# Kernel optimization log

Hardware: AMD Instinct MI355X
Metric: run time of the kernel (lower is better)

The kernel has to match this reference:

```python
import jax, jax.numpy as jnp
import numpy as np

THRESHOLD = 0.2
NEG_POS_RATIO = 3
ALPHA = 1.0
B, M, P, C = 64, 50, 24564, 2


def cxcy_to_xy(c):
    return jnp.concatenate([c[..., :2] - c[..., 2:] / 2, c[..., :2] + c[..., 2:] / 2], axis=-1)


def xy_to_cxcy(x):
    return jnp.concatenate([(x[..., :2] + x[..., 2:]) / 2, x[..., 2:] - x[..., :2]], axis=-1)


def cxcy_to_gcxgcy(c, p):
    # SSD encoding: offsets scaled by 10, sizes (log) scaled by 5
    return jnp.concatenate([(c[..., :2] - p[..., :2]) / (p[..., 2:] / 10.0),
                            jnp.log(c[..., 2:] / p[..., 2:]) * 5.0], axis=-1)


def jaccard(a, b):
    # a: (M,4) xy boxes, b: (P,4) xy boxes -> (M,P) IoU
    lt = jnp.maximum(a[:, None, :2], b[None, :, :2])
    rb = jnp.minimum(a[:, None, 2:], b[None, :, 2:])
    inter = jnp.prod(jnp.clip(rb - lt, 0.0), axis=-1)
    area_a = jnp.prod(a[:, 2:] - a[:, :2], axis=-1)
    area_b = jnp.prod(b[:, 2:] - b[:, :2], axis=-1)
    return inter / (area_a[:, None] + area_b[None, :] - inter)


def setup_inputs() -> dict:
    key = jax.random.key(0)
    k1, k2, k3, k4, k5, k6 = jax.random.split(key, 6)
    predicted_locs = jax.random.normal(k1, (B, P, 4), dtype=jnp.float32)
    predicted_scores = jax.random.normal(k2, (B, P, C), dtype=jnp.float32)
    # valid GT corner boxes in [0,1]: x2>x1, y2>y1
    xy1 = jax.random.uniform(k3, (B, M, 2), minval=0.0, maxval=0.75)
    wh = jax.random.uniform(k4, (B, M, 2), minval=0.05, maxval=0.25)
    boxes = jnp.concatenate([xy1, xy1 + wh], axis=-1).astype(jnp.float32)
    # priors in cxcywh with positive sizes
    pc = jax.random.uniform(k5, (P, 2), minval=0.0, maxval=1.0)
    pwh = jax.random.uniform(k6, (P, 2), minval=0.02, maxval=0.3)
    priors_cxcy = jnp.concatenate([pc, pwh], axis=-1).astype(jnp.float32)
    return {"predicted_locs": predicted_locs, "predicted_scores": predicted_scores,
            "boxes": boxes, "priors_cxcy": priors_cxcy}


def reference(predicted_locs, predicted_scores, boxes, priors_cxcy):
    n_priors = priors_cxcy.shape[0]
    priors_xy = cxcy_to_xy(priors_cxcy)

    def assign(boxes_i):  # boxes_i: (M,4) xy
        overlap = jaccard(boxes_i, priors_xy)  # (M,P)
        overlap_for_each_prior = overlap.max(axis=0)        # (P,)
        object_for_each_prior = overlap.argmax(axis=0)      # (P,)
        prior_for_each_object = overlap.argmax(axis=1)      # (M,)
        # force each object's best prior to be assigned to that object
        object_for_each_prior = object_for_each_prior.at[prior_for_each_object].set(jnp.arange(boxes_i.shape[0]))
        overlap_for_each_prior = overlap_for_each_prior.at[prior_for_each_object].set(1.0)
        labels = jnp.where(overlap_for_each_prior < THRESHOLD, 0, 1).astype(jnp.int32)
        true_locs = cxcy_to_gcxgcy(xy_to_cxcy(boxes_i[object_for_each_prior]), priors_cxcy)
        return labels, true_locs

    true_classes, true_locs = jax.vmap(assign)(boxes)  # (B,P), (B,P,4)
    pos = true_classes != 0                            # (B,P)
    n_pos = pos.sum(axis=1)                            # (B,)
    total_pos = n_pos.sum().astype(jnp.float32)

    # L1Loss(mean) over the positive-prior coordinates
    loc_abs = jnp.abs(predicted_locs - true_locs)
    loc_loss = jnp.sum(loc_abs * pos[..., None]) / (total_pos * 4.0)

    # per-prior cross entropy
    logp = jax.nn.log_softmax(predicted_scores, axis=-1)
    conf_all = -jnp.take_along_axis(logp, true_classes[..., None].astype(jnp.int32), axis=-1)[..., 0]  # (B,P)
    conf_pos_sum = jnp.sum(conf_all * pos)

    # hard negative mining: zero positives, sort descending, take top 3*n_pos per image
    conf_neg = jnp.where(pos, 0.0, conf_all)
    conf_neg_sorted = -jnp.sort(-conf_neg, axis=1)
    ranks = jnp.arange(n_priors)[None, :]
    hard = ranks < (NEG_POS_RATIO * n_pos)[:, None]
    conf_hard_sum = jnp.sum(conf_neg_sorted * hard)

    conf_loss = (conf_hard_sum + conf_pos_sum) / total_pos
    return conf_loss + ALPHA * loc_loss
```

## Files before the change

### kernel.cpp

```cpp
#include <hip/hip_runtime.h>
#include <math.h>

#define BB 64
#define MM 50
#define PP 24564
#define CC 2
#define NBLK ((PP + 255) / 256)
#define THRESH 0.2f
#define P4 (PP / 4)
#define MCH 5
#define MGRID (MM / MCH)

__global__ void k_priors(const float4* __restrict__ pr_cxcy,
                         float4* __restrict__ pr_xy,
                         float* __restrict__ parea,
                         int* __restrict__ ghist) {
    int p = blockIdx.x * 256 + threadIdx.x;
    for (int i = p; i < BB * 2048; i += NBLK * 256) ghist[i] = 0;
    if (p >= PP) return;
    float4 c = pr_cxcy[p];
    float4 xy;
    xy.x = c.x - c.z * 0.5f;
    xy.y = c.y - c.w * 0.5f;
    xy.z = c.x + c.z * 0.5f;
    xy.w = c.y + c.w * 0.5f;
    pr_xy[p] = xy;
    parea[p] = (xy.z - xy.x) * (xy.w - xy.y);
}

__global__ void k_best_per_object(const float4* __restrict__ pr_xy,
                                  const float* __restrict__ parea,
                                  const float4* __restrict__ boxes,
                                  int* __restrict__ pfeo) {
    int b = blockIdx.y;
    int m0 = blockIdx.x * MCH;
    int tid = threadIdx.x;
    float4 bx[MCH];
    float ba[MCH];
    #pragma unroll
    for (int j = 0; j < MCH; ++j) {
        bx[j] = boxes[b * MM + m0 + j];
        ba[j] = (bx[j].z - bx[j].x) * (bx[j].w - bx[j].y);
    }
    float bi[MCH], bd[MCH];
    int bp[MCH];
    #pragma unroll
    for (int j = 0; j < MCH; ++j) { bi[j] = 0.0f; bd[j] = 1.0f; bp[j] = 0; }
    for (int p = tid; p < PP; p += 256) {
        float4 pxy = pr_xy[p];
        float pa = parea[p];
        #pragma unroll
        for (int j = 0; j < MCH; ++j) {
            float lx = fmaxf(bx[j].x, pxy.x), ly = fmaxf(bx[j].y, pxy.y);
            float rx = fminf(bx[j].z, pxy.z), ry = fminf(bx[j].w, pxy.w);
            float iw = fmaxf(rx - lx, 0.0f), ih = fmaxf(ry - ly, 0.0f);
            float inter = iw * ih;
            float den = ba[j] + pa - inter;
            float l = inter * bd[j], r = bi[j] * den;
            if (l > r) { bi[j] = inter; bd[j] = den; bp[j] = p; }
        }
    }
    __shared__ float sI[256], sD[256];
    __shared__ int sP[256];
    for (int j = 0; j < MCH; ++j) {
        sI[tid] = bi[j]; sD[tid] = bd[j]; sP[tid] = bp[j];
        __syncthreads();
        for (int s = 128; s > 0; s >>= 1) {
            if (tid < s) {
                float l = sI[tid + s] * sD[tid], r = sI[tid] * sD[tid + s];
                if (l > r || (l == r && sP[tid + s] < sP[tid])) {
                    sI[tid] = sI[tid + s]; sD[tid] = sD[tid + s]; sP[tid] = sP[tid + s];
                }
            }
            __syncthreads();
        }
        if (tid == 0) pfeo[b * MM + m0 + j] = sP[0];
        __syncthreads();
    }
}

__global__ void k_fused(const float4* __restrict__ pr_xy,
                        const float* __restrict__ parea,
                        const float4* __restrict__ boxes,
                        const int* __restrict__ pfeo,
                        const float4* __restrict__ pr_cxcy,
                        const float4* __restrict__ plocs,
                        const float2* __restrict__ scores,
                        float* __restrict__ confneg,
                        int* __restrict__ ghist,
                        int* __restrict__ npos_part,
                        float* __restrict__ cpos_part,
                        float* __restrict__ loc_part) {
    int b = blockIdx.y;
    int p = blockIdx.x * 256 + threadIdx.x;
    int tid = threadIdx.x;
    __shared__ float4 sbox[MM];
    __shared__ float sarea[MM];
    __shared__ int spfeo[MM];
    __shared__ int shist[2048];
    __shared__ int si[256];
    __shared__ float s1[256], s2[256];
    for (int i = tid; i < 2048; i += 256) shist[i] = 0;
    if (tid < MM) {
        float4 bx = boxes[b * MM + tid];
        sbox[tid] = bx;
        sarea[tid] = (bx.z - bx.x) * (bx.w - bx.y);
        spfeo[tid] = pfeo[b * MM + tid];
    }
    __syncthreads();

    int np = 0;
    float cpos = 0.0f, lloc = 0.0f;
    if (p < PP) {
        float4 pxy = pr_xy[p];
        float pa = parea[p];
        float binter = 0.0f, bdenom = 1.0f;
        int bm = 0;
        for (int m = 0; m < MM; ++m) {
            float4 bxm = sbox[m];
            float lx = fmaxf(bxm.x, pxy.x), ly = fmaxf(bxm.y, pxy.y);
            float rx = fminf(bxm.z, pxy.z), ry = fminf(bxm.w, pxy.w);
            float iw = fmaxf(rx - lx, 0.0f), ih = fmaxf(ry - ly, 0.0f);
            float inter = iw * ih;
            float den = sarea[m] + pa - inter;
            float l = inter * bdenom, r = binter * den;
            if (l > r) { binter = inter; bdenom = den; bm = m; }
        }
        float best = binter / bdenom;
        for (int m = 0; m < MM; ++m) {
            if (spfeo[m] == p) { bm = m; best = 1.0f; }
        }
        bool pos = (best >= THRESH);
        size_t idx = (size_t)b * PP + p;
        float2 sc = scores[idx];
        float mx = fmaxf(sc.x, sc.y);
        float lse = mx + logf(expf(sc.x - mx) + expf(sc.y - mx));
        float conf = pos ? (lse - sc.y) : (lse - sc.x);
        float key = pos ? 0.0f : conf;
        confneg[idx] = key;
        atomicAdd(&shist[__float_as_uint(key) >> 20], 1);
        if (pos) {
            np = 1;
            cpos = conf;
            float4 bx = sbox[bm];
            float cx = (bx.x + bx.z) * 0.5f, cy = (bx.y + bx.w) * 0.5f;
            float w = bx.z - bx.x, h = bx.w - bx.y;
            float4 pc = pr_cxcy[p];
            float g0 = (cx - pc.x) / (pc.z * 0.1f);
            float g1 = (cy - pc.y) / (pc.w * 0.1f);
            float g2 = logf(w / pc.z) * 5.0f;
            float g3 = logf(h / pc.w) * 5.0f;
            float4 pl = plocs[idx];
            lloc = fabsf(pl.x - g0) + fabsf(pl.y - g1) +
                   fabsf(pl.z - g2) + fabsf(pl.w - g3);
        }
    }
    si[tid] = np; s1[tid] = cpos; s2[tid] = lloc;
    __syncthreads();
    for (int s = 128; s > 0; s >>= 1) {
        if (tid < s) {
            si[tid] += si[tid + s];
            s1[tid] += s1[tid + s];
            s2[tid] += s2[tid + s];
        }
        __syncthreads();
    }
    if (tid == 0) {
        int o = b * NBLK + blockIdx.x;
        npos_part[o] = si[0];
        cpos_part[o] = s1[0];
        loc_part[o] = s2[0];
    }
    for (int i = tid; i < 2048; i += 256) {
        int c = shist[i];
        if (c) atomicAdd(&ghist[b * 2048 + i], c);
    }
}

__device__ __forceinline__ float block_sum(float v, float* fred, int tid) {
    fred[tid] = v;
    __syncthreads();
    for (int s = 128; s > 0; s >>= 1) {
        if (tid < s) fred[tid] += fred[tid + s];
        __syncthreads();
    }
    float r = fred[0];
    __syncthreads();
    return r;
}

template <int NB>
__device__ __forceinline__ void suffix_find(const int* __restrict__ h, int K, int tid,
                                            int* iscr, int* bcast, int slot) {
    const int c = NB / 256;
    const int base = tid * c;
    int tsum = 0;
    #pragma unroll
    for (int i = 0; i < c; ++i) tsum += h[base + i];
    iscr[tid] = tsum;
    __syncthreads();
    int val = tsum;
    for (int off = 1; off < 256; off <<= 1) {
        int other = (tid + off < 256) ? iscr[tid + off] : 0;
        __syncthreads();
        val += other;
        iscr[tid] = val;
        __syncthreads();
    }
    int acc = val - tsum;
    int best = -1, cg = 0;
    for (int i = base + c - 1; i >= base; --i) {
        int s = acc + h[i];
        if (s >= K) { best = i; cg = acc; break; }
        acc = s;
    }
    iscr[tid] = best;
    __syncthreads();
    for (int s2 = 128; s2 > 0; s2 >>= 1) {
        if (tid < s2) iscr[tid] = max(iscr[tid], iscr[tid + s2]);
        __syncthreads();
    }
    int gbest = iscr[0];
    __syncthreads();
    if (best == gbest && best >= 0) { bcast[slot] = gbest; bcast[slot + 1] = cg; }
    __syncthreads();
}

__global__ void k_select(const float* __restrict__ confneg,
                         const int* __restrict__ ghist,
                         const int* __restrict__ npos_part,
                         float* __restrict__ chard) {
    int b = blockIdx.x, tid = threadIdx.x;
    __shared__ int h[2048];
    __shared__ float store[4096];
    __shared__ float fred[256];
    __shared__ int iscr[256];
    __shared__ int bcast[8];

    iscr[tid] = (tid < NBLK) ? npos_part[b * NBLK + tid] : 0;
    __syncthreads();
    for (int s = 128; s > 0; s >>= 1) {
        if (tid < s) iscr[tid] += iscr[tid + s];
        __syncthreads();
    }
    int npos = iscr[0];
    __syncthreads();
    long long Kl = 3LL * npos;
    int K = (Kl > PP) ? PP : (int)Kl;
    if (K == 0) {
        if (tid == 0) chard[b] = 0.0f;
        return;
    }

    for (int i = tid; i < 2048; i += 256) h[i] = ghist[b * 2048 + i];
    __syncthreads();
    suffix_find<2048>(h, K, tid, iscr, bcast, 0);
    int b1 = bcast[0];
    int K1 = K - bcast[1];
    int h1cnt = h[b1];
    bool docollect = (h1cnt <= 4096);
    __syncthreads();

    for (int i = tid; i < 1024; i += 256) h[i] = 0;
    if (tid == 0) bcast[6] = 0;
    __syncthreads();
    const float4* cn4 = (const float4*)(confneg + (size_t)b * PP);
    float sa = 0.0f;
    for (int i = tid; i < P4; i += 256) {
        float4 q = cn4[i];
        float vv[4] = {q.x, q.y, q.z, q.w};
        #pragma unroll
        for (int j = 0; j < 4; ++j) {
            unsigned k = __float_as_uint(vv[j]);
            int t11 = (int)(k >> 20);
            if (t11 > b1) sa += vv[j];
            else if (t11 == b1) {
                atomicAdd(&h[(k >> 10) & 1023], 1);
                if (docollect) {
                    int ix = atomicAdd(&bcast[6], 1);
                    store[ix] = vv[j];
                }
            }
        }
    }
    float Sa = block_sum(sa, fred, tid);
    suffix_find<1024>(h, K1, tid, iscr, bcast, 2);
    int b2 = bcast[2];
    int K2 = K1 - bcast[3];
    unsigned top21 = ((unsigned)b1 << 10) | (unsigned)b2;
    __syncthreads();

    float Sb, Sc;
    int b3, K3;
    if (docollect) {
        for (int i = tid; i < 1024; i += 256) h[i] = 0;
        __syncthreads();
        float sb = 0.0f;
        for (int i = tid; i < h1cnt; i += 256) {
            unsigned k = __float_as_uint(store[i]);
            int n10 = (int)((k >> 10) & 1023);
            if (n10 > b2) sb += store[i];
            else if (n10 == b2) atomicAdd(&h[k & 1023], 1);
        }
        Sb = block_sum(sb, fred, tid);
        suffix_find<1024>(h, K2, tid, iscr, bcast, 4);
        b3 = bcast[4];
        K3 = K2 - bcast[5];
        float sc = 0.0f;
        for (int i = tid; i < h1cnt; i += 256) {
            unsigned k = __float_as_uint(store[i]);
            if ((k >> 10) == top21 && (k & 1023) > (unsigned)b3) sc += store[i];
        }
        Sc = block_sum(sc, fred, tid);
    } else {
        for (int i = tid; i < 1024; i += 256) h[i] = 0;
        __syncthreads();
        float sb = 0.0f;
        for (int i = tid; i < P4; i += 256) {
            float4 q = cn4[i];
            float vv[4] = {q.x, q.y, q.z, q.w};
            #pragma unroll
            for (int j = 0; j < 4; ++j) {
                unsigned k = __float_as_uint(vv[j]);
                if ((int)(k >> 20) == b1) {
                    int n10 = (int)((k >> 10) & 1023);
                    if (n10 > b2) sb += vv[j];
                    else if (n10 == b2) atomicAdd(&h[k & 1023], 1);
                }
            }
        }
        Sb = block_sum(sb, fred, tid);
        suffix_find<1024>(h, K2, tid, iscr, bcast, 4);
        b3 = bcast[4];
        K3 = K2 - bcast[5];
        float sc = 0.0f;
        for (int i = tid; i < P4; i += 256) {
            float4 q = cn4[i];
            float vv[4] = {q.x, q.y, q.z, q.w};
            #pragma unroll
            for (int j = 0; j < 4; ++j) {
                unsigned k = __float_as_uint(vv[j]);
                if ((k >> 10) == top21 && (k & 1023) > (unsigned)b3) sc += vv[j];
            }
        }
        Sc = block_sum(sc, fred, tid);
    }
    if (tid == 0) {
        unsigned kstar = (top21 << 10) | (unsigned)b3;
        chard[b] = Sa + Sb + Sc + (float)K3 * __uint_as_float(kstar);
    }
}

__global__ void k_final(const int* __restrict__ npos_part,
                        const float* __restrict__ cpos_part,
                        const float* __restrict__ loc_part,
                        const float* __restrict__ chard,
                        float* __restrict__ out) {
    __shared__ int si[256];
    __shared__ float s1[256], s2[256], s3[256];
    int tn = 0; float tc = 0.0f, tl = 0.0f;
    for (int i = threadIdx.x; i < BB * NBLK; i += 256) {
        tn += npos_part[i];
        tc += cpos_part[i];
        tl += loc_part[i];
    }
    float th = (threadIdx.x < BB) ? chard[threadIdx.x] : 0.0f;
    si[threadIdx.x] = tn; s1[threadIdx.x] = tc; s2[threadIdx.x] = tl; s3[threadIdx.x] = th;
    __syncthreads();
    for (int s = 128; s > 0; s >>= 1) {
        if (threadIdx.x < s) {
            si[threadIdx.x] += si[threadIdx.x + s];
            s1[threadIdx.x] += s1[threadIdx.x + s];
            s2[threadIdx.x] += s2[threadIdx.x + s];
            s3[threadIdx.x] += s3[threadIdx.x + s];
        }
        __syncthreads();
    }
    if (threadIdx.x == 0) {
        float tp = (float)si[0];
        out[0] = (s3[0] + s1[0]) / tp + s2[0] / (tp * 4.0f);
    }
}

extern "C" void kernel_launch(void* const* d_in, const int* in_sizes, int n_in,
                              void* d_out, int out_size, void* d_ws, size_t ws_size,
                              hipStream_t stream) {
    const float4* plocs   = (const float4*)d_in[0];
    const float2* scores  = (const float2*)d_in[1];
    const float4* boxes   = (const float4*)d_in[2];
    const float4* priors  = (const float4*)d_in[3];
    float* out = (float*)d_out;

    char* ws = (char*)d_ws;
    size_t off = 0;
    auto alloc = [&](size_t bytes) -> void* {
        void* p = ws + off;
        off += (bytes + 255) & ~(size_t)255;
        return p;
    };
    float4* pr_xy    = (float4*)alloc((size_t)PP * 16);
    float*  parea    = (float*) alloc((size_t)PP * 4);
    int*    pfeo     = (int*)   alloc((size_t)BB * MM * 4);
    float*  confneg  = (float*) alloc((size_t)BB * PP * 4);
    int*    ghist    = (int*)   alloc((size_t)BB * 2048 * 4);
    int*    npos_p   = (int*)   alloc((size_t)BB * NBLK * 4);
    float*  cpos_p   = (float*) alloc((size_t)BB * NBLK * 4);
    float*  loc_p    = (float*) alloc((size_t)BB * NBLK * 4);
    float*  chard    = (float*) alloc((size_t)BB * 4);
    (void)ws_size; (void)in_sizes; (void)n_in; (void)out_size;

    k_priors<<<dim3(NBLK), 256, 0, stream>>>(priors, pr_xy, parea, ghist);
    k_best_per_object<<<dim3(MGRID, BB), 256, 0, stream>>>(pr_xy, parea, boxes, pfeo);
    k_fused<<<dim3(NBLK, BB), 256, 0, stream>>>(pr_xy, parea, boxes, pfeo, priors,
                                                plocs, scores, confneg, ghist,
                                                npos_p, cpos_p, loc_p);
    k_select<<<BB, 256, 0, stream>>>(confneg, ghist, npos_p, chard);
    k_final<<<1, 256, 0, stream>>>(npos_p, cpos_p, loc_p, chard, out);
}
```

Measured before the change: 160.3 us.

## Split best-prior-per-object search across prior chunks with packed 64-bit atomicMax

Splits the argmax over priors for each ground-truth object into 8 prior chunks across a new grid dimension, giving more blocks. Each block reduces within a wavefront using shuffles and merges partial winners with a 64-bit atomicMax on a key of (IoU bits, inverted prior index). The shared-memory tree reduction and its barriers go away, and each block now handles 10 objects instead of 5. The per-wave atomic merge relies on the IoU being computed by division, which can differ slightly from the cross-multiplied comparison and change tie handling. The key buffer is zeroed in the prior kernel.

```diff
diff --git a/kernel.cpp b/kernel.cpp
--- a/kernel.cpp
+++ b/kernel.cpp
@@ -8,15 +8,19 @@
 #define NBLK ((PP + 255) / 256)
 #define THRESH 0.2f
 #define P4 (PP / 4)
-#define MCH 5
+#define MCH 10
 #define MGRID (MM / MCH)
+#define NC 8
+#define PCHUNK ((PP + NC - 1) / NC)
 
 __global__ void k_priors(const float4* __restrict__ pr_cxcy,
                          float4* __restrict__ pr_xy,
                          float* __restrict__ parea,
-                         int* __restrict__ ghist) {
+                         int* __restrict__ ghist,
+                         unsigned long long* __restrict__ pfeo64) {
     int p = blockIdx.x * 256 + threadIdx.x;
     for (int i = p; i < BB * 2048; i += NBLK * 256) ghist[i] = 0;
+    if (p < BB * MM) pfeo64[p] = 0ull;
     if (p >= PP) return;
     float4 c = pr_cxcy[p];
     float4 xy;
@@ -31,10 +35,13 @@
 __global__ void k_best_per_object(const float4* __restrict__ pr_xy,
                                   const float* __restrict__ parea,
                                   const float4* __restrict__ boxes,
-                                  int* __restrict__ pfeo) {
-    int b = blockIdx.y;
+                                  unsigned long long* __restrict__ pfeo64) {
+    int b = blockIdx.z;
     int m0 = blockIdx.x * MCH;
+    int c = blockIdx.y;
     int tid = threadIdx.x;
+    int pstart = c * PCHUNK;
+    int pend = min(pstart + PCHUNK, PP);
     float4 bx[MCH];
     float ba[MCH];
     #pragma unroll
@@ -46,7 +53,7 @@
     int bp[MCH];
     #pragma unroll
     for (int j = 0; j < MCH; ++j) { bi[j] = 0.0f; bd[j] = 1.0f; bp[j] = 0; }
-    for (int p = tid; p < PP; p += 256) {
+    for (int p = pstart + tid; p < pend; p += 256) {
         float4 pxy = pr_xy[p];
         float pa = parea[p];
         #pragma unroll
@@ -60,29 +67,31 @@
             if (l > r) { bi[j] = inter; bd[j] = den; bp[j] = p; }
         }
     }
-    __shared__ float sI[256], sD[256];
-    __shared__ int sP[256];
+    #pragma unroll
     for (int j = 0; j < MCH; ++j) {
-        sI[tid] = bi[j]; sD[tid] = bd[j]; sP[tid] = bp[j];
-        __syncthreads();
-        for (int s = 128; s > 0; s >>= 1) {
-            if (tid < s) {
-                float l = sI[tid + s] * sD[tid], r = sI[tid] * sD[tid + s];
-                if (l > r || (l == r && sP[tid + s] < sP[tid])) {
-                    sI[tid] = sI[tid + s]; sD[tid] = sD[tid + s]; sP[tid] = sP[tid + s];
-                }
-            }
-            __syncthreads();
-        }
-        if (tid == 0) pfeo[b * MM + m0 + j] = sP[0];
-        __syncthreads();
+        float I = bi[j], D = bd[j];
+        int P_ = bp[j];
+        #pragma unroll
+        for (int off = 32; off > 0; off >>= 1) {
+            float oI = __shfl_xor(I, off);
+            float oD = __shfl_xor(D, off);
+            int oP = __shfl_xor(P_, off);
+            float l = oI * D, r = I * oD;
+            if (l > r || (l == r && oP < P_)) { I = oI; D = oD; P_ = oP; }
+        }
+        if ((tid & 63) == 0) {
+            float q = I / D;
+            unsigned long long key =
+                ((unsigned long long)__float_as_uint(q) << 32) | (unsigned int)(~P_);
+            atomicMax(&pfeo64[b * MM + m0 + j], key);
+        }
     }
 }
 
 __global__ void k_fused(const float4* __restrict__ pr_xy,
                         const float* __restrict__ parea,
                         const float4* __restrict__ boxes,
-                        const int* __restrict__ pfeo,
+                        const unsigned long long* __restrict__ pfeo64,
                         const float4* __restrict__ pr_cxcy,
                         const float4* __restrict__ plocs,
                         const float2* __restrict__ scores,
@@ -105,7 +114,7 @@
         float4 bx = boxes[b * MM + tid];
         sbox[tid] = bx;
         sarea[tid] = (bx.z - bx.x) * (bx.w - bx.y);
-        spfeo[tid] = pfeo[b * MM + tid];
+        spfeo[tid] = (int)(~(unsigned int)(pfeo64[b * MM + tid] & 0xFFFFFFFFull));
     }
     __syncthreads();
 
@@ -398,20 +407,20 @@
         off += (bytes + 255) & ~(size_t)255;
         return p;
     };
-    float4* pr_xy    = (float4*)alloc((size_t)PP * 16);
-    float*  parea    = (float*) alloc((size_t)PP * 4);
-    int*    pfeo     = (int*)   alloc((size_t)BB * MM * 4);
-    float*  confneg  = (float*) alloc((size_t)BB * PP * 4);
-    int*    ghist    = (int*)   alloc((size_t)BB * 2048 * 4);
-    int*    npos_p   = (int*)   alloc((size_t)BB * NBLK * 4);
-    float*  cpos_p   = (float*) alloc((size_t)BB * NBLK * 4);
-    float*  loc_p    = (float*) alloc((size_t)BB * NBLK * 4);
-    float*  chard    = (float*) alloc((size_t)BB * 4);
+    float4*             pr_xy   = (float4*)alloc((size_t)PP * 16);
+    float*              parea   = (float*) alloc((size_t)PP * 4);
+    unsigned long long* pfeo64  = (unsigned long long*)alloc((size_t)BB * MM * 8);
+    float*              confneg = (float*) alloc((size_t)BB * PP * 4);
+    int*                ghist   = (int*)   alloc((size_t)BB * 2048 * 4);
+    int*                npos_p  = (int*)   alloc((size_t)BB * NBLK * 4);
+    float*              cpos_p  = (float*) alloc((size_t)BB * NBLK * 4);
+    float*              loc_p   = (float*) alloc((size_t)BB * NBLK * 4);
+    float*              chard   = (float*) alloc((size_t)BB * 4);
     (void)ws_size; (void)in_sizes; (void)n_in; (void)out_size;
 
-    k_priors<<<dim3(NBLK), 256, 0, stream>>>(priors, pr_xy, parea, ghist);
-    k_best_per_object<<<dim3(MGRID, BB), 256, 0, stream>>>(pr_xy, parea, boxes, pfeo);
-    k_fused<<<dim3(NBLK, BB), 256, 0, stream>>>(pr_xy, parea, boxes, pfeo, priors,
+    k_priors<<<dim3(NBLK), 256, 0, stream>>>(priors, pr_xy, parea, ghist, pfeo64);
+    k_best_per_object<<<dim3(MGRID, NC, BB), 256, 0, stream>>>(pr_xy, parea, boxes, pfeo64);
+    k_fused<<<dim3(NBLK, BB), 256, 0, stream>>>(pr_xy, parea, boxes, pfeo64, priors,
                                                 plocs, scores, confneg, ghist,
                                                 npos_p, cpos_p, loc_p);
     k_select<<<BB, 256, 0, stream>>>(confneg, ghist, npos_p, chard);
```

Result: no change. 159.0 us (-0.8%).
